# Kernel tuning notes

Measured on AMD Instinct MI355X. Metric: run time of the kernel, lower is better.

Reference implementation:

```python
import jax, jax.numpy as jnp
import numpy as np

COMMITMENT_COST = 0.25
NUM_EMBEDDINGS = 1024
EMBEDDING_DIM = 64


def setup_inputs() -> dict:
    key = jax.random.key(0)
    k1, k2 = jax.random.split(key)
    z = jax.random.normal(k1, (32, EMBEDDING_DIM, 64, 64), dtype=jnp.float32)
    # nn.Embedding init: uniform(-1/K, 1/K)
    lim = 1.0 / NUM_EMBEDDINGS
    embeddings = jax.random.uniform(k2, (NUM_EMBEDDINGS, EMBEDDING_DIM),
                                    dtype=jnp.float32, minval=-lim, maxval=lim)
    return {"z": z, "embeddings": embeddings}


def reference(z, embeddings):
    # z: [B, C, H, W] with C == embedding_dim
    B, C, H, W = z.shape
    z_perm = jnp.transpose(z, (0, 2, 3, 1))          # [B, H, W, C]
    flat_z = z_perm.reshape(-1, C)                    # [N, C]

    # squared L2 distances: ||z||^2 - 2 z.E^T + ||E||^2  -> [N, K]
    distances = (jnp.sum(flat_z * flat_z, axis=1, keepdims=True)
                 - 2.0 * flat_z @ embeddings.T
                 + jnp.sum(embeddings * embeddings, axis=1))
    encoding_indices = jnp.argmin(distances, axis=1)  # [N]

    # direct gather (equivalent to one-hot @ embeddings)
    quantized = embeddings[encoding_indices].reshape(z_perm.shape)  # [B,H,W,C]

    commitment_loss = COMMITMENT_COST * jnp.mean(
        (jax.lax.stop_gradient(quantized) - z_perm) ** 2)
    codebook_loss = jnp.mean((quantized - jax.lax.stop_gradient(z_perm)) ** 2)
    loss = commitment_loss + codebook_loss

    # straight-through estimator
    quantized_st = z_perm + jax.lax.stop_gradient(quantized - z_perm)
    out = jnp.transpose(quantized_st, (0, 3, 1, 2))   # [B, C, H, W]
    return out, loss
```

## Files before the change

kernel.cpp:

```cpp
#include <hip/hip_runtime.h>
#include <hip/hip_bf16.h>

#define CDIM   64
#define HWDIM  4096
#define NCODES 1024
#define NELEM  8388608
#define NBLOCK 256
#define NPART  (NBLOCK * 16)
#define LDSSZ  (131072 + 16 * 68 * 4)

typedef short bf16x8 __attribute__((ext_vector_type(8)));
typedef float f32x4  __attribute__((ext_vector_type(4)));

__device__ __forceinline__ unsigned short f2bf(float f) {
    union { float f; unsigned u; } v; v.f = f;
    unsigned r = v.u + 0x7fffu + ((v.u >> 16) & 1u);
    return (unsigned short)(r >> 16);
}
__device__ __forceinline__ unsigned asu(float f) {
    union { float f; unsigned u; } v; v.f = f; return v.u;
}
__device__ __forceinline__ float asf(unsigned u) {
    union { unsigned u; float f; } v; v.u = u; return v.f;
}

__global__ __launch_bounds__(1024)
void vq_main(const float* __restrict__ z,
             const float* __restrict__ E,
             float* __restrict__ out,
             float* __restrict__ partial) {
    extern __shared__ char smem[];
    unsigned short* sEb = (unsigned short*)smem;
    float (*sBiasT)[68] = (float(*)[68])(smem + 131072);

    const int lane = threadIdx.x & 63;
    const int wave = threadIdx.x >> 6;
    const int lrow = lane & 15;
    const int lgrp = lane >> 4;

    const int n0 = blockIdx.x * 512 + wave * 32;
    const int b  = n0 >> 12;
    const int hw = n0 & 4095;
    const float* zb   = z   + (size_t)b * (CDIM * HWDIM);
    float*       outb = out + (size_t)b * (CDIM * HWDIM);

    float zv[32];
    #pragma unroll
    for (int t = 0; t < 2; ++t)
        #pragma unroll
        for (int s = 0; s < 2; ++s)
            #pragma unroll
            for (int j = 0; j < 8; ++j)
                zv[t * 16 + s * 8 + j] =
                    zb[(32 * s + 8 * lgrp + j) * HWDIM + hw + t * 16 + lrow];

    {
        const int t = threadIdx.x;
        const float4* ev = (const float4*)(E + t * CDIM);
        float s = 0.f;
        #pragma unroll
        for (int k = 0; k < 8; ++k) {
            float4 va = ev[2 * k], vb = ev[2 * k + 1];
            s = fmaf(va.x, va.x, s); s = fmaf(va.y, va.y, s);
            s = fmaf(va.z, va.z, s); s = fmaf(va.w, va.w, s);
            s = fmaf(vb.x, vb.x, s); s = fmaf(vb.y, vb.y, s);
            s = fmaf(vb.z, vb.z, s); s = fmaf(vb.w, vb.w, s);
            bf16x8 w;
            w[0] = (short)f2bf(va.x); w[1] = (short)f2bf(va.y);
            w[2] = (short)f2bf(va.z); w[3] = (short)f2bf(va.w);
            w[4] = (short)f2bf(vb.x); w[5] = (short)f2bf(vb.y);
            w[6] = (short)f2bf(vb.z); w[7] = (short)f2bf(vb.w);
            *(bf16x8*)((char*)sEb + t * 128 + ((k ^ (t & 7)) << 4)) = w;
        }
        sBiasT[t & 15][t >> 4] = -0.5f * s;
    }

    float szz = 0.f;
    bf16x8 afrag[2][2];
    #pragma unroll
    for (int t = 0; t < 2; ++t)
        #pragma unroll
        for (int s = 0; s < 2; ++s)
            #pragma unroll
            for (int j = 0; j < 8; ++j) {
                float v = zv[t * 16 + s * 8 + j];
                szz = fmaf(v, v, szz);
                afrag[t][s][j] = (short)f2bf(v);
            }

    float run[2][4];
    #pragma unroll
    for (int t = 0; t < 2; ++t)
        #pragma unroll
        for (int r = 0; r < 4; ++r) run[t][r] = -3.0e38f;

    __syncthreads();

    const int s0byte = (lgrp ^ (lrow & 7)) << 4;
    const char* pa = (const char*)sEb + lrow * 128 + s0byte;
    const char* pb = (const char*)sEb + lrow * 128 + (s0byte ^ 64);
    const float* pbias = &sBiasT[lrow][0];
    unsigned codev = (unsigned)lrow;

    for (int ch = 0; ch < 8; ++ch) {
        f32x4 bq0 = *(const f32x4*)(pbias);
        f32x4 bq1 = *(const f32x4*)(pbias + 4);
        #pragma unroll
        for (int j = 0; j < 8; ++j) {
            bf16x8 b0 = *(const bf16x8*)(pa + j * 2048);
            bf16x8 b1 = *(const bf16x8*)(pb + j * 2048);
            const float bv = (j < 4) ? bq0[j] : bq1[j - 4];
            f32x4 ci = {bv, bv, bv, bv};
            f32x4 a0 = __builtin_amdgcn_mfma_f32_16x16x32_bf16(afrag[0][0], b0, ci, 0, 0, 0);
            a0 = __builtin_amdgcn_mfma_f32_16x16x32_bf16(afrag[0][1], b1, a0, 0, 0, 0);
            f32x4 a1 = __builtin_amdgcn_mfma_f32_16x16x32_bf16(afrag[1][0], b0, ci, 0, 0, 0);
            a1 = __builtin_amdgcn_mfma_f32_16x16x32_bf16(afrag[1][1], b1, a1, 0, 0, 0);
            const unsigned code = codev + (unsigned)(j * 16);
            #pragma unroll
            for (int r = 0; r < 4; ++r) {
                float k0 = asf((asu(a0[r]) & 0xFFFFFC00u) | code);
                run[0][r] = fmaxf(run[0][r], k0);
                float k1 = asf((asu(a1[r]) & 0xFFFFFC00u) | code);
                run[1][r] = fmaxf(run[1][r], k1);
            }
        }
        pa += 16384; pb += 16384; pbias += 8; codev += 128;
    }

    #pragma unroll
    for (int m = 1; m <= 8; m <<= 1)
        #pragma unroll
        for (int t = 0; t < 2; ++t)
            #pragma unroll
            for (int r = 0; r < 4; ++r)
                run[t][r] = fmaxf(run[t][r], __shfl_xor(run[t][r], m, 64));

    int idxe[2];
    #pragma unroll
    for (int t = 0; t < 2; ++t) {
        const int src = (lrow >> 2) << 4;
        float g0 = __shfl(run[t][0], src, 64);
        float g1 = __shfl(run[t][1], src, 64);
        float g2 = __shfl(run[t][2], src, 64);
        float g3 = __shfl(run[t][3], src, 64);
        float sel = (lrow & 2) ? ((lrow & 1) ? g3 : g2)
                               : ((lrow & 1) ? g1 : g0);
        idxe[t] = (int)(asu(sel) & 1023u);
    }

    #pragma unroll
    for (int t = 0; t < 2; ++t) {
        const int idxr = idxe[t];
        const f32x4* ep  = (const f32x4*)(E + idxr * CDIM      + 8 * lgrp);
        const f32x4* ep2 = (const f32x4*)(E + idxr * CDIM + 32 + 8 * lgrp);
        f32x4 qa = ep[0], qb = ep[1], qc = ep2[0], qd = ep2[1];
        float* ob = outb + hw + t * 16 + lrow;
        #pragma unroll
        for (int j = 0; j < 4; ++j) {
            ob[(8 * lgrp + j)          * HWDIM] = qa[j];
            ob[(8 * lgrp + 4 + j)      * HWDIM] = qb[j];
            ob[(32 + 8 * lgrp + j)     * HWDIM] = qc[j];
            ob[(32 + 8 * lgrp + 4 + j) * HWDIM] = qd[j];
        }
    }

    float dsum = 0.f;
    #pragma unroll
    for (int t = 0; t < 2; ++t)
        #pragma unroll
        for (int r = 0; r < 4; ++r) dsum += run[t][r];
    float contrib = szz + ((lrow == 0) ? (-2.f * dsum) : 0.f);
    #pragma unroll
    for (int m = 32; m >= 1; m >>= 1) contrib += __shfl_xor(contrib, m, 64);
    if (lane == 0) partial[blockIdx.x * 16 + wave] = contrib;
}

__global__ __launch_bounds__(1024)
void vq_fin(const float* __restrict__ partial,
            float* __restrict__ out) {
    __shared__ float red[16];
    const int tid = threadIdx.x;
    float s = 0.f;
    #pragma unroll
    for (int i = 0; i < NPART / 1024; ++i) s += partial[i * 1024 + tid];
    #pragma unroll
    for (int m = 32; m >= 1; m >>= 1) s += __shfl_xor(s, m, 64);
    if ((tid & 63) == 0) red[tid >> 6] = s;
    __syncthreads();
    if (tid == 0) {
        float tot = 0.f;
        #pragma unroll
        for (int w = 0; w < 16; ++w) tot += red[w];
        out[NELEM] = 1.25f * tot / (float)NELEM;
    }
}

extern "C" void kernel_launch(void* const* d_in, const int* in_sizes, int n_in,
                              void* d_out, int out_size, void* d_ws, size_t ws_size,
                              hipStream_t stream) {
    const float* z = (const float*)d_in[0];
    const float* E = (const float*)d_in[1];
    float* out = (float*)d_out;
    float* partial = (float*)d_ws;

    hipFuncSetAttribute((const void*)vq_main,
                        hipFuncAttributeMaxDynamicSharedMemorySize, LDSSZ);

    vq_main<<<NBLOCK, 1024, LDSSZ, stream>>>(z, E, out, partial);
    vq_fin<<<1, 1024, 0, stream>>>(partial, out);
}
```

Measured before the change: 36.96 us.

## Use FP8 MFMA distances with a prep kernel and async LDS codebook staging

Converts the codebook once in a separate prep kernel into scaled FP8 plus precomputed norm biases, and loads it into LDS with global_load_lds. The main kernel then computes distances with fp8 MFMA on 16 points per wave, using 512-thread blocks and four times as many blocks. The aim is to halve codebook LDS traffic, remove the per-block codebook conversion, and raise occupancy. In exchange it adds a kernel launch and loses precision: FP8 rounding of z and the codebook can change argmin choices and the loss value.

```diff
diff --git a/kernel.cpp b/kernel.cpp
--- a/kernel.cpp
+++ b/kernel.cpp
@@ -5,100 +5,121 @@
 #define HWDIM  4096
 #define NCODES 1024
 #define NELEM  8388608
-#define NBLOCK 256
-#define NPART  (NBLOCK * 16)
-#define LDSSZ  (131072 + 16 * 68 * 4)
-
-typedef short bf16x8 __attribute__((ext_vector_type(8)));
-typedef float f32x4  __attribute__((ext_vector_type(4)));
-
-__device__ __forceinline__ unsigned short f2bf(float f) {
-    union { float f; unsigned u; } v; v.f = f;
-    unsigned r = v.u + 0x7fffu + ((v.u >> 16) & 1u);
-    return (unsigned short)(r >> 16);
-}
+#define NBLOCK 1024
+#define NPART  (NBLOCK * 8)
+#define LDSSZ  (65536 + 16 * 68 * 4)
+
+typedef float f32x4 __attribute__((ext_vector_type(4)));
+
 __device__ __forceinline__ unsigned asu(float f) {
     union { float f; unsigned u; } v; v.f = f; return v.u;
 }
 __device__ __forceinline__ float asf(unsigned u) {
     union { unsigned u; float f; } v; v.u = u; return v.f;
 }
-
-__global__ __launch_bounds__(1024)
+__device__ __forceinline__ void gload_lds16(const void* g, void* l) {
+    __builtin_amdgcn_global_load_lds(
+        (const __attribute__((address_space(1))) void*)g,
+        (__attribute__((address_space(3))) void*)l, 16, 0, 0);
+}
+
+__global__ void vq_prep(const float* __restrict__ E,
+                        unsigned char* __restrict__ Eb,
+                        float* __restrict__ biasS) {
+    int t = blockIdx.x * blockDim.x + threadIdx.x;
+    if (t < NCODES) {
+        const float4* ev = (const float4*)(E + t * CDIM);
+        float s = 0.f;
+        int dw[16];
+        #pragma unroll
+        for (int i = 0; i < 16; ++i) {
+            float4 v = ev[i];
+            s = fmaf(v.x, v.x, s); s = fmaf(v.y, v.y, s);
+            s = fmaf(v.z, v.z, s); s = fmaf(v.w, v.w, s);
+            int d = __builtin_amdgcn_cvt_pk_fp8_f32(v.x * 16384.f, v.y * 16384.f, 0, false);
+            d     = __builtin_amdgcn_cvt_pk_fp8_f32(v.z * 16384.f, v.w * 16384.f, d, true);
+            dw[i] = d;
+        }
+        int4* dst = (int4*)(Eb + t * CDIM);
+        #pragma unroll
+        for (int k = 0; k < 4; ++k) {
+            int4 q; q.x = dw[4*k]; q.y = dw[4*k+1]; q.z = dw[4*k+2]; q.w = dw[4*k+3];
+            dst[k] = q;
+        }
+        biasS[t] = -8192.f * s;
+    }
+}
+
+__global__ __launch_bounds__(512)
 void vq_main(const float* __restrict__ z,
              const float* __restrict__ E,
+             const unsigned char* __restrict__ Eb,
+             const float* __restrict__ biasS,
              float* __restrict__ out,
              float* __restrict__ partial) {
     extern __shared__ char smem[];
-    unsigned short* sEb = (unsigned short*)smem;
-    float (*sBiasT)[68] = (float(*)[68])(smem + 131072);
+    unsigned char* sEb = (unsigned char*)smem;
+    float (*sBiasT)[68] = (float(*)[68])(smem + 65536);
 
     const int lane = threadIdx.x & 63;
     const int wave = threadIdx.x >> 6;
     const int lrow = lane & 15;
     const int lgrp = lane >> 4;
 
-    const int n0 = blockIdx.x * 512 + wave * 32;
+    const int n0 = blockIdx.x * 128 + wave * 16;
     const int b  = n0 >> 12;
     const int hw = n0 & 4095;
     const float* zb   = z   + (size_t)b * (CDIM * HWDIM);
     float*       outb = out + (size_t)b * (CDIM * HWDIM);
 
-    float zv[32];
-    #pragma unroll
-    for (int t = 0; t < 2; ++t)
-        #pragma unroll
-        for (int s = 0; s < 2; ++s)
-            #pragma unroll
-            for (int j = 0; j < 8; ++j)
-                zv[t * 16 + s * 8 + j] =
-                    zb[(32 * s + 8 * lgrp + j) * HWDIM + hw + t * 16 + lrow];
-
-    {
-        const int t = threadIdx.x;
-        const float4* ev = (const float4*)(E + t * CDIM);
-        float s = 0.f;
-        #pragma unroll
-        for (int k = 0; k < 8; ++k) {
-            float4 va = ev[2 * k], vb = ev[2 * k + 1];
-            s = fmaf(va.x, va.x, s); s = fmaf(va.y, va.y, s);
-            s = fmaf(va.z, va.z, s); s = fmaf(va.w, va.w, s);
-            s = fmaf(vb.x, vb.x, s); s = fmaf(vb.y, vb.y, s);
-            s = fmaf(vb.z, vb.z, s); s = fmaf(vb.w, vb.w, s);
-            bf16x8 w;
-            w[0] = (short)f2bf(va.x); w[1] = (short)f2bf(va.y);
-            w[2] = (short)f2bf(va.z); w[3] = (short)f2bf(va.w);
-            w[4] = (short)f2bf(vb.x); w[5] = (short)f2bf(vb.y);
-            w[6] = (short)f2bf(vb.z); w[7] = (short)f2bf(vb.w);
-            *(bf16x8*)((char*)sEb + t * 128 + ((k ^ (t & 7)) << 4)) = w;
-        }
-        sBiasT[t & 15][t >> 4] = -0.5f * s;
+    #pragma unroll
+    for (int i = 0; i < 8; ++i) {
+        const int cid = i * 512 + (int)threadIdx.x;
+        const int row = cid >> 2;
+        const int s16 = cid & 3;
+        const unsigned char* g = Eb + row * CDIM + ((s16 ^ (row & 3)) << 4);
+        gload_lds16(g, sEb + cid * 16);
+    }
+    {
+        const int i = (int)threadIdx.x;
+        sBiasT[i & 15][i >> 4] = biasS[i];
+        const int i2 = i + 512;
+        sBiasT[i2 & 15][i2 >> 4] = biasS[i2];
     }
 
     float szz = 0.f;
-    bf16x8 afrag[2][2];
-    #pragma unroll
-    for (int t = 0; t < 2; ++t)
-        #pragma unroll
-        for (int s = 0; s < 2; ++s)
-            #pragma unroll
-            for (int j = 0; j < 8; ++j) {
-                float v = zv[t * 16 + s * 8 + j];
-                szz = fmaf(v, v, szz);
-                afrag[t][s][j] = (short)f2bf(v);
-            }
-
-    float run[2][4];
-    #pragma unroll
-    for (int t = 0; t < 2; ++t)
-        #pragma unroll
-        for (int r = 0; r < 4; ++r) run[t][r] = -3.0e38f;
+    long a0, a1;
+    {
+        float zv[8];
+        #pragma unroll
+        for (int j = 0; j < 8; ++j) {
+            float v = zb[(8 * lgrp + j) * HWDIM + hw + lrow];
+            szz = fmaf(v, v, szz); zv[j] = v;
+        }
+        int dlo = __builtin_amdgcn_cvt_pk_fp8_f32(zv[0], zv[1], 0, false);
+        dlo     = __builtin_amdgcn_cvt_pk_fp8_f32(zv[2], zv[3], dlo, true);
+        int dhi = __builtin_amdgcn_cvt_pk_fp8_f32(zv[4], zv[5], 0, false);
+        dhi     = __builtin_amdgcn_cvt_pk_fp8_f32(zv[6], zv[7], dhi, true);
+        a0 = (long)(unsigned)dlo | ((long)dhi << 32);
+        #pragma unroll
+        for (int j = 0; j < 8; ++j) {
+            float v = zb[(32 + 8 * lgrp + j) * HWDIM + hw + lrow];
+            szz = fmaf(v, v, szz); zv[j] = v;
+        }
+        dlo = __builtin_amdgcn_cvt_pk_fp8_f32(zv[0], zv[1], 0, false);
+        dlo = __builtin_amdgcn_cvt_pk_fp8_f32(zv[2], zv[3], dlo, true);
+        dhi = __builtin_amdgcn_cvt_pk_fp8_f32(zv[4], zv[5], 0, false);
+        dhi = __builtin_amdgcn_cvt_pk_fp8_f32(zv[6], zv[7], dhi, true);
+        a1 = (long)(unsigned)dlo | ((long)dhi << 32);
+    }
+
+    float run[4] = {-3.0e38f, -3.0e38f, -3.0e38f, -3.0e38f};
 
     __syncthreads();
 
-    const int s0byte = (lgrp ^ (lrow & 7)) << 4;
-    const char* pa = (const char*)sEb + lrow * 128 + s0byte;
-    const char* pb = (const char*)sEb + lrow * 128 + (s0byte ^ 64);
+    const int ch0 = (((lgrp >> 1) ^ (lrow & 3)) << 4) + ((lgrp & 1) << 3);
+    const char* pa = (const char*)sEb + lrow * 64 + ch0;
+    const char* pb = (const char*)sEb + lrow * 64 + (ch0 ^ 32);
     const float* pbias = &sBiasT[lrow][0];
     unsigned codev = (unsigned)lrow;
 
@@ -107,54 +128,44 @@
         f32x4 bq1 = *(const f32x4*)(pbias + 4);
         #pragma unroll
         for (int j = 0; j < 8; ++j) {
-            bf16x8 b0 = *(const bf16x8*)(pa + j * 2048);
-            bf16x8 b1 = *(const bf16x8*)(pb + j * 2048);
+            long b0 = *(const long*)(pa + j * 1024);
+            long b1 = *(const long*)(pb + j * 1024);
             const float bv = (j < 4) ? bq0[j] : bq1[j - 4];
             f32x4 ci = {bv, bv, bv, bv};
-            f32x4 a0 = __builtin_amdgcn_mfma_f32_16x16x32_bf16(afrag[0][0], b0, ci, 0, 0, 0);
-            a0 = __builtin_amdgcn_mfma_f32_16x16x32_bf16(afrag[0][1], b1, a0, 0, 0, 0);
-            f32x4 a1 = __builtin_amdgcn_mfma_f32_16x16x32_bf16(afrag[1][0], b0, ci, 0, 0, 0);
-            a1 = __builtin_amdgcn_mfma_f32_16x16x32_bf16(afrag[1][1], b1, a1, 0, 0, 0);
+            f32x4 acc = __builtin_amdgcn_mfma_f32_16x16x32_fp8_fp8(a0, b0, ci, 0, 0, 0);
+            acc = __builtin_amdgcn_mfma_f32_16x16x32_fp8_fp8(a1, b1, acc, 0, 0, 0);
             const unsigned code = codev + (unsigned)(j * 16);
             #pragma unroll
-            for (int r = 0; r < 4; ++r) {
-                float k0 = asf((asu(a0[r]) & 0xFFFFFC00u) | code);
-                run[0][r] = fmaxf(run[0][r], k0);
-                float k1 = asf((asu(a1[r]) & 0xFFFFFC00u) | code);
-                run[1][r] = fmaxf(run[1][r], k1);
-            }
-        }
-        pa += 16384; pb += 16384; pbias += 8; codev += 128;
+            for (int r = 0; r < 4; ++r)
+                run[r] = fmaxf(run[r], asf((asu(acc[r]) & 0xFFFFFC00u) | code));
+        }
+        pa += 8192; pb += 8192; pbias += 8; codev += 128;
     }
 
     #pragma unroll
     for (int m = 1; m <= 8; m <<= 1)
         #pragma unroll
-        for (int t = 0; t < 2; ++t)
-            #pragma unroll
-            for (int r = 0; r < 4; ++r)
-                run[t][r] = fmaxf(run[t][r], __shfl_xor(run[t][r], m, 64));
-
-    int idxe[2];
-    #pragma unroll
-    for (int t = 0; t < 2; ++t) {
+        for (int r = 0; r < 4; ++r)
+            run[r] = fmaxf(run[r], __shfl_xor(run[r], m, 64));
+
+    int idxe;
+    float kmine;
+    {
         const int src = (lrow >> 2) << 4;
-        float g0 = __shfl(run[t][0], src, 64);
-        float g1 = __shfl(run[t][1], src, 64);
-        float g2 = __shfl(run[t][2], src, 64);
-        float g3 = __shfl(run[t][3], src, 64);
-        float sel = (lrow & 2) ? ((lrow & 1) ? g3 : g2)
-                               : ((lrow & 1) ? g1 : g0);
-        idxe[t] = (int)(asu(sel) & 1023u);
-    }
-
-    #pragma unroll
-    for (int t = 0; t < 2; ++t) {
-        const int idxr = idxe[t];
-        const f32x4* ep  = (const f32x4*)(E + idxr * CDIM      + 8 * lgrp);
-        const f32x4* ep2 = (const f32x4*)(E + idxr * CDIM + 32 + 8 * lgrp);
+        float g0 = __shfl(run[0], src, 64);
+        float g1 = __shfl(run[1], src, 64);
+        float g2 = __shfl(run[2], src, 64);
+        float g3 = __shfl(run[3], src, 64);
+        kmine = (lrow & 2) ? ((lrow & 1) ? g3 : g2)
+                           : ((lrow & 1) ? g1 : g0);
+        idxe = (int)(asu(kmine) & 1023u);
+    }
+
+    {
+        const f32x4* ep  = (const f32x4*)(E + idxe * CDIM      + 8 * lgrp);
+        const f32x4* ep2 = (const f32x4*)(E + idxe * CDIM + 32 + 8 * lgrp);
         f32x4 qa = ep[0], qb = ep[1], qc = ep2[0], qd = ep2[1];
-        float* ob = outb + hw + t * 16 + lrow;
+        float* ob = outb + hw + lrow;
         #pragma unroll
         for (int j = 0; j < 4; ++j) {
             ob[(8 * lgrp + j)          * HWDIM] = qa[j];
@@ -164,15 +175,11 @@
         }
     }
 
-    float dsum = 0.f;
-    #pragma unroll
-    for (int t = 0; t < 2; ++t)
-        #pragma unroll
-        for (int r = 0; r < 4; ++r) dsum += run[t][r];
-    float contrib = szz + ((lrow == 0) ? (-2.f * dsum) : 0.f);
+    float dsum = run[0] + run[1] + run[2] + run[3];
+    float contrib = szz + ((lrow == 0) ? (-1.220703125e-4f * dsum) : 0.f);
     #pragma unroll
     for (int m = 32; m >= 1; m >>= 1) contrib += __shfl_xor(contrib, m, 64);
-    if (lane == 0) partial[blockIdx.x * 16 + wave] = contrib;
+    if (lane == 0) partial[blockIdx.x * 8 + wave] = contrib;
 }
 
 __global__ __launch_bounds__(1024)
@@ -201,11 +208,15 @@
     const float* z = (const float*)d_in[0];
     const float* E = (const float*)d_in[1];
     float* out = (float*)d_out;
-    float* partial = (float*)d_ws;
+
+    unsigned char* Eb = (unsigned char*)d_ws;
+    float* biasS      = (float*)((char*)d_ws + 65536);
+    float* partial    = (float*)((char*)d_ws + 65536 + 4096);
 
     hipFuncSetAttribute((const void*)vq_main,
                         hipFuncAttributeMaxDynamicSharedMemorySize, LDSSZ);
 
-    vq_main<<<NBLOCK, 1024, LDSSZ, stream>>>(z, E, out, partial);
+    vq_prep<<<4, 256, 0, stream>>>(E, Eb, biasS);
+    vq_main<<<NBLOCK, 512, LDSSZ, stream>>>(z, E, Eb, biasS, out, partial);
     vq_fin<<<1, 1024, 0, stream>>>(partial, out);
 }
```

New measurement: 50.11 us. 1.36x slower.
